# Optimization experiments

Hardware: AMD Instinct MI355X
Metric: run time of the kernel (lower is better)

The kernel has to match this reference:

```python
import jax, jax.numpy as jnp
import numpy as np

B, S, D, H = 2, 2048, 1024, 16
HD = D // H  # 64
NEG = 1.0e9


def setup_inputs() -> dict:
    key = jax.random.key(0)
    ks = jax.random.split(key, 9)
    scale = 1.0 / np.sqrt(D)
    return {
        "q_in": jax.random.normal(ks[0], (B, S, D), jnp.float32),
        "k_in": jax.random.normal(ks[1], (B, S, D), jnp.float32),
        "v_in": jax.random.normal(ks[2], (B, S, D), jnp.float32),
        "Wq": jax.random.normal(ks[3], (D, D), jnp.float32) * scale,
        "bq": jnp.zeros((D,), jnp.float32),
        "Wk": jax.random.normal(ks[4], (D, D), jnp.float32) * scale,
        "bk": jnp.zeros((D,), jnp.float32),
        "Wv": jax.random.normal(ks[5], (D, D), jnp.float32) * scale,
        "bv": jnp.zeros((D,), jnp.float32),
        "Wo": jax.random.normal(ks[6], (D, D), jnp.float32) * scale,
        "bo": jnp.zeros((D,), jnp.float32),
    }


def _split_heads(x):
    # [B,S,D] -> [B,H,S,HD]
    return x.reshape(B, S, H, HD).transpose(0, 2, 1, 3)


def reference(q_in, k_in, v_in, Wq, bq, Wk, bk, Wv, bv, Wo, bo):
    q = _split_heads(q_in @ Wq + bq)
    k = _split_heads(k_in @ Wk + bk)
    v = _split_heads(v_in @ Wv + bv)
    # scaled dot-product attention with additive causal mask (use_causal_mask=True)
    scores = jnp.einsum("bhqd,bhkd->bhqk", q, k) / jnp.sqrt(jnp.float32(HD))
    causal = jnp.tril(jnp.ones((S, S), jnp.float32))  # band_part(ones, -1, 0)
    scores = scores + (causal - 1.0) * NEG
    weights = jax.nn.softmax(scores, axis=-1)
    attn = jnp.einsum("bhqk,bhkd->bhqd", weights, v)
    concat = attn.transpose(0, 2, 1, 3).reshape(B, S, D)
    return concat @ Wo + bo
```

## Files before the change

### kernel.cpp

```cpp
#include <hip/hip_runtime.h>

#define B_  2
#define S_  2048
#define D_  1024
#define H_  16
#define HD_ 64
#define MM  (B_ * S_)

typedef __bf16 bf16;
typedef __attribute__((ext_vector_type(8))) __bf16 bf16x8;
typedef __attribute__((ext_vector_type(4))) __bf16 bf16x4;
typedef __attribute__((ext_vector_type(4))) float  f32x4;

__device__ inline float exp2g(float x) { return __builtin_amdgcn_exp2f(x); }

__device__ inline bf16x8 load8(const bf16* p) { return *(const bf16x8*)p; }
__device__ inline bf16x8 load8(const float* p) {
  float4 a = *(const float4*)p;
  float4 b = *(const float4*)(p + 4);
  bf16x8 r;
  r[0] = (bf16)a.x; r[1] = (bf16)a.y; r[2] = (bf16)a.z; r[3] = (bf16)a.w;
  r[4] = (bf16)b.x; r[5] = (bf16)b.y; r[6] = (bf16)b.z; r[7] = (bf16)b.w;
  return r;
}

__device__ inline void gld16(void* lds, const void* g) {
  __builtin_amdgcn_global_load_lds(
      (const __attribute__((address_space(1))) unsigned int*)g,
      (__attribute__((address_space(3))) unsigned int*)lds, 16, 0, 0);
}

__global__ __launch_bounds__(256) void transpose_w(
    const float* __restrict__ W0, const float* __restrict__ W1,
    const float* __restrict__ W2, const float* __restrict__ W3,
    bf16* __restrict__ T0, bf16* __restrict__ T1,
    bf16* __restrict__ T2, bf16* __restrict__ T3,
    const float* __restrict__ X0, const float* __restrict__ X1,
    const float* __restrict__ X2,
    bf16* __restrict__ Y0, bf16* __restrict__ Y1, bf16* __restrict__ Y2) {
  const int z = blockIdx.z;
  if (z >= 4) {
    const int p = z - 4, t = p >> 2;
    const float* src = t == 0 ? X0 : t == 1 ? X1 : X2;
    bf16* dst = t == 0 ? Y0 : t == 1 ? Y1 : Y2;
    long base = ((long)(p & 3) << 20) +
                (long)(blockIdx.y * 32 + blockIdx.x) * 1024 + threadIdx.x * 4;
    float4 v = *(const float4*)&src[base];
    bf16x4 o4;
    o4[0] = (bf16)v.x; o4[1] = (bf16)v.y; o4[2] = (bf16)v.z; o4[3] = (bf16)v.w;
    *(bf16x4*)&dst[base] = o4;
    return;
  }
  __shared__ bf16 t[32][40];
  const float* in = z == 0 ? W0 : z == 1 ? W1 : z == 2 ? W2 : W3;
  bf16* out = z == 0 ? T0 : z == 1 ? T1 : z == 2 ? T2 : T3;
  const int tx = threadIdx.x & 31;
  const int ty = threadIdx.x >> 5;
  const int r0 = blockIdx.y * 32, c0 = blockIdx.x * 32;
#pragma unroll
  for (int j = 0; j < 32; j += 8)
    t[ty + j][tx] = (bf16)in[(long)(r0 + ty + j) * D_ + (c0 + tx)];
  __syncthreads();
#pragma unroll
  for (int j = 0; j < 32; j += 8)
    out[(long)(c0 + ty + j) * D_ + (r0 + tx)] = t[tx][ty + j];
}

__global__ __launch_bounds__(256) void transpose_v64(const bf16* __restrict__ V,
                                                     bf16* __restrict__ VT) {
  __shared__ bf16 t[64][72];
  const int tid = threadIdx.x;
  const int s0 = blockIdx.x * 64;
  const int bh = blockIdx.y;
  const int b = bh >> 4, h = bh & 15;
  const bf16* ip = V + (long)b * S_ * D_ + h * HD_;
  bf16* op = VT + (long)bh * HD_ * S_;
#pragma unroll
  for (int i = 0; i < 2; ++i) {
    int c = tid + i * 256;
    int r = c >> 3, cc = (c & 7) * 8;
    *(bf16x8*)&t[r][cc] = *(const bf16x8*)&ip[(long)(s0 + r) * D_ + cc];
  }
  __syncthreads();
#pragma unroll
  for (int i = 0; i < 2; ++i) {
    int c = tid + i * 256;
    int d = c >> 3, sc = (c & 7) * 8;
    bf16x8 v;
#pragma unroll
    for (int j = 0; j < 8; ++j) v[j] = t[sc + j][d];
    *(bf16x8*)&op[(long)d * S_ + s0 + sc] = v;
  }
}

template <typename AT, typename OT>
__global__ __launch_bounds__(256) void gemm_bt_dma(
    const AT* __restrict__ A0, const AT* __restrict__ A1, const AT* __restrict__ A2,
    const bf16* __restrict__ B0, const bf16* __restrict__ B1, const bf16* __restrict__ B2,
    const float* __restrict__ c0, const float* __restrict__ c1, const float* __restrict__ c2,
    OT* __restrict__ C0, OT* __restrict__ C1, OT* __restrict__ C2,
    int M, int N, int K) {
  __shared__ bf16 lA[128][32];
  __shared__ bf16 lB[128][32];
  const int z = blockIdx.z;
  const AT*    A    = z == 0 ? A0 : z == 1 ? A1 : A2;
  const bf16*  Bt   = z == 0 ? B0 : z == 1 ? B1 : B2;
  const float* bias = z == 0 ? c0 : z == 1 ? c1 : c2;
  OT*          C    = z == 0 ? C0 : z == 1 ? C1 : C2;

  const int tid = threadIdx.x;
  const int lane = tid & 63, wave = tid >> 6;
  const int quad = lane >> 4, l16 = lane & 15;
  const int bm = blockIdx.y * 128, bn = blockIdx.x * 128;
  const int wm = (wave >> 1) * 64, wn = (wave & 1) * 64;

  f32x4 acc[4][4] = {};

  for (int k0 = 0; k0 < K; k0 += 32) {
    __syncthreads();
#pragma unroll
    for (int i = 0; i < 2; ++i) {
      const int nbase = wave * 128 + i * 64;
      const int n = nbase + lane;
      const int row = n >> 2, kc = (n & 3) * 8;
      gld16(&lB[0][0] + (long)nbase * 8, &Bt[(long)(bn + row) * K + k0 + kc]);
      if constexpr (__is_same(AT, bf16))
        gld16(&lA[0][0] + (long)nbase * 8, &A[(long)(bm + row) * K + k0 + kc]);
    }
    if constexpr (!__is_same(AT, bf16)) {
#pragma unroll
      for (int i = 0; i < 2; ++i) {
        int c = tid + i * 256;
        int row = c >> 2, kc = (c & 3) * 8;
        *(bf16x8*)&lA[row][kc] = load8(&A[(long)(bm + row) * K + k0 + kc]);
      }
    }
    __syncthreads();
    bf16x8 af[4], bfr[4];
#pragma unroll
    for (int i = 0; i < 4; ++i) {
      af[i]  = *(const bf16x8*)&lA[wm + i * 16 + l16][quad * 8];
      bfr[i] = *(const bf16x8*)&lB[wn + i * 16 + l16][quad * 8];
    }
#pragma unroll
    for (int mi = 0; mi < 4; ++mi)
#pragma unroll
      for (int ni = 0; ni < 4; ++ni)
        acc[mi][ni] = __builtin_amdgcn_mfma_f32_16x16x32_bf16(af[mi], bfr[ni],
                                                              acc[mi][ni], 0, 0, 0);
  }

#pragma unroll
  for (int mi = 0; mi < 4; ++mi)
#pragma unroll
    for (int ni = 0; ni < 4; ++ni) {
      int col = bn + wn + ni * 16 + l16;
      float bv = bias[col];
#pragma unroll
      for (int r = 0; r < 4; ++r) {
        int row = bm + wm + mi * 16 + quad * 4 + r;
        C[(long)row * N + col] = (OT)(acc[mi][ni][r] + bv);
      }
    }
}

__global__ __launch_bounds__(256) void gemm_bt_64(const bf16* __restrict__ A,
                                                  const bf16* __restrict__ Bt,
                                                  const float* __restrict__ bias,
                                                  float* __restrict__ C,
                                                  int M, int N, int K) {
  __shared__ bf16 lA[128][32];
  __shared__ bf16 lB[64][32];
  const int tid = threadIdx.x;
  const int lane = tid & 63, wave = tid >> 6;
  const int quad = lane >> 4, l16 = lane & 15;
  const int bm = blockIdx.y * 128, bn = blockIdx.x * 64;
  const int wm = (wave >> 1) * 64, wn = (wave & 1) * 32;

  f32x4 acc[4][2] = {};

  for (int k0 = 0; k0 < K; k0 += 32) {
    __syncthreads();
#pragma unroll
    for (int i = 0; i < 2; ++i) {
      const int nbase = wave * 128 + i * 64;
      const int n = nbase + lane;
      const int row = n >> 2, kc = (n & 3) * 8;
      gld16(&lA[0][0] + (long)nbase * 8, &A[(long)(bm + row) * K + k0 + kc]);
    }
    {
      const int nbase = wave * 64;
      const int n = nbase + lane;
      const int row = n >> 2, kc = (n & 3) * 8;
      gld16(&lB[0][0] + (long)nbase * 8, &Bt[(long)(bn + row) * K + k0 + kc]);
    }
    __syncthreads();
    bf16x8 af[4], bfr[2];
#pragma unroll
    for (int i = 0; i < 4; ++i)
      af[i] = *(const bf16x8*)&lA[wm + i * 16 + l16][quad * 8];
#pragma unroll
    for (int i = 0; i < 2; ++i)
      bfr[i] = *(const bf16x8*)&lB[wn + i * 16 + l16][quad * 8];
#pragma unroll
    for (int mi = 0; mi < 4; ++mi)
#pragma unroll
      for (int ni = 0; ni < 2; ++ni)
        acc[mi][ni] = __builtin_amdgcn_mfma_f32_16x16x32_bf16(af[mi], bfr[ni],
                                                              acc[mi][ni], 0, 0, 0);
  }

#pragma unroll
  for (int mi = 0; mi < 4; ++mi)
#pragma unroll
    for (int ni = 0; ni < 2; ++ni) {
      int col = bn + wn + ni * 16 + l16;
      float bv = bias[col];
#pragma unroll
      for (int r = 0; r < 4; ++r) {
        int row = bm + wm + mi * 16 + quad * 4 + r;
        C[(long)row * N + col] = acc[mi][ni][r] + bv;
      }
    }
}

#define SCALE_LOG2E 0.1803368801111244f

__device__ inline void attn_step7(bool diag, int qloc, int kh, int quad,
                                  int l16,
                                  const bf16 (*lKb)[64], const bf16 (*lVb)[64],
                                  bf16 (*lpw)[72], const bf16x8* aq,
                                  f32x4* o, float& l_s) {
  const int sw = l16 & 7;
  f32x4 s[2];
#pragma unroll
  for (int i = 0; i < 2; ++i) {
    const int ni = 2 * kh + i;
    f32x4 a = {};
#pragma unroll
    for (int c = 0; c < 2; ++c) {
      bf16x8 kf = *(const bf16x8*)&lKb[ni * 16 + l16][((c * 4 + quad) ^ sw) * 8];
      a = __builtin_amdgcn_mfma_f32_16x16x32_bf16(kf, aq[c], a, 0, 0, 0);
    }
    s[i] = a * SCALE_LOG2E;
  }
  if (diag) {
#pragma unroll
    for (int i = 0; i < 2; ++i)
#pragma unroll
      for (int r = 0; r < 4; ++r)
        if ((2 * kh + i) * 16 + quad * 4 + r > qloc) s[i][r] = -1e9f;
  }
  float rs = 0.f;
#pragma unroll
  for (int i = 0; i < 2; ++i) {
    bf16x4 p4;
#pragma unroll
    for (int r = 0; r < 4; ++r) {
      float p = exp2g(s[i][r]);
      p4[r] = (bf16)p;
      rs += p;
    }
    *(bf16x4*)&lpw[l16][(2 * kh + i) * 16 + quad * 4] = p4;
  }
  l_s += rs;
  bf16x8 ap = *(const bf16x8*)&lpw[l16][kh * 32 + quad * 8];
#pragma unroll
  for (int di = 0; di < 4; ++di) {
    bf16x8 vf = *(const bf16x8*)&lVb[di * 16 + l16][((kh * 4 + quad) ^ sw) * 8];
    o[di] = __builtin_amdgcn_mfma_f32_16x16x32_bf16(vf, ap, o[di], 0, 0, 0);
  }
}

__device__ inline void store_o(bf16* Ob, int qrow, int lane, int quad, int l16,
                               bf16 (*lpw)[72], const f32x4* o, float l_s) {
  float rs = l_s;
  rs += __shfl_xor(rs, 16);
  rs += __shfl_xor(rs, 32);
  const float inv = 1.0f / rs;
#pragma unroll
  for (int di = 0; di < 4; ++di) {
    bf16x4 p4;
#pragma unroll
    for (int r = 0; r < 4; ++r) p4[r] = (bf16)(o[di][r] * inv);
    *(bf16x4*)&lpw[l16][di * 16 + quad * 4] = p4;
  }
  const int q = lane >> 2, db = (lane & 3) * 16;
  bf16x8 v0 = *(const bf16x8*)&lpw[q][db];
  bf16x8 v1 = *(const bf16x8*)&lpw[q][db + 8];
  *(bf16x8*)&Ob[(long)(qrow + q) * D_ + db] = v0;
  *(bf16x8*)&Ob[(long)(qrow + q) * D_ + db + 8] = v1;
}

__global__ __launch_bounds__(512) void flash_attn7(const bf16* __restrict__ Q,
                                                   const bf16* __restrict__ K,
                                                   const bf16* __restrict__ VT,
                                                   bf16* __restrict__ O) {
  __shared__ bf16 lKV[2][2][64][64];
  __shared__ bf16 lp[8][16][72];
  __shared__ float lsum[512];
  const int tid = threadIdx.x;
  const int lane = tid & 63, wave = tid >> 6;
  const int quad = lane >> 4, l16 = lane & 15;
  const int qgroup = wave & 3, kh = wave >> 2;
  const int x = blockIdx.x, bh = blockIdx.y;
  const int qtA = x, qtB = 31 - x;
  const int b = bh >> 4, h = bh & 15;
  const bf16* Qb = Q + (long)b * S_ * D_ + h * HD_;
  const bf16* Kb = K + (long)b * S_ * D_ + h * HD_;
  const bf16* Vb = VT + (long)bh * HD_ * S_;
  const int qrowA = qtA * 64 + qgroup * 16;
  const int qrowB = qtB * 64 + qgroup * 16;
  const int qloc = qgroup * 16 + l16;

  bf16x8 aqA[2], aqB[2];
#pragma unroll
  for (int c = 0; c < 2; ++c) {
    aqA[c] = *(const bf16x8*)&Qb[(long)(qrowA + l16) * D_ + c * 32 + quad * 8];
    aqB[c] = *(const bf16x8*)&Qb[(long)(qrowB + l16) * D_ + c * 32 + quad * 8];
  }

  f32x4 oA[4] = {}, oB[4] = {};
  float lA = 0.f, lB = 0.f;

  const int srow = tid >> 3, scol = tid & 7;
  const int swcol = (scol ^ (srow & 7)) * 8;

  bf16x8 kreg, vreg;
  kreg = *(const bf16x8*)&Kb[(long)srow * D_ + scol * 8];
  vreg = *(const bf16x8*)&Vb[(long)srow * S_ + scol * 8];
  *(bf16x8*)&lKV[0][0][srow][swcol] = kreg;
  *(bf16x8*)&lKV[1][0][srow][swcol] = vreg;
  __syncthreads();

  for (int t = 0; t <= 32; ++t) {
    const int p = t & 1;
    if (t < 32) {
      const int g = (t + 1 <= qtA) ? (t + 1) : (t - qtA);
      const long k0 = (long)g * 64;
      kreg = *(const bf16x8*)&Kb[(k0 + srow) * D_ + scol * 8];
      vreg = *(const bf16x8*)&Vb[(long)srow * S_ + k0 + scol * 8];
    }
    if (t <= qtA)
      attn_step7(t == qtA, qloc, kh, quad, l16, lKV[0][p], lKV[1][p],
                 lp[qgroup], aqA, oA, lA);
    else
      attn_step7(t == 32, qloc, kh, quad, l16, lKV[0][p], lKV[1][p],
                 lp[qgroup], aqB, oB, lB);
    if (t < 32) {
      *(bf16x8*)&lKV[0][1 - p][srow][swcol] = kreg;
      *(bf16x8*)&lKV[1][1 - p][srow][swcol] = vreg;
      __syncthreads();
    }
  }

  __syncthreads();
  float* scrO = (float*)lKV;
  const int pairid = qgroup * 64 + lane;
  if (kh == 1) {
#pragma unroll
    for (int di = 0; di < 4; ++di)
#pragma unroll
      for (int r = 0; r < 4; ++r)
        scrO[pairid * 16 + di * 4 + r] = oA[di][r];
    lsum[pairid] = lA;
  } else {
#pragma unroll
    for (int di = 0; di < 4; ++di)
#pragma unroll
      for (int r = 0; r < 4; ++r)
        scrO[4096 + pairid * 16 + di * 4 + r] = oB[di][r];
    lsum[256 + pairid] = lB;
  }
  __syncthreads();
  bf16* Ob = O + (long)b * S_ * D_ + h * HD_;
  if (kh == 0) {
#pragma unroll
    for (int di = 0; di < 4; ++di)
#pragma unroll
      for (int r = 0; r < 4; ++r)
        oA[di][r] += scrO[pairid * 16 + di * 4 + r];
    lA += lsum[pairid];
    store_o(Ob, qrowA, lane, quad, l16, lp[wave], oA, lA);
  } else {
#pragma unroll
    for (int di = 0; di < 4; ++di)
#pragma unroll
      for (int r = 0; r < 4; ++r)
        oB[di][r] += scrO[4096 + pairid * 16 + di * 4 + r];
    lB += lsum[256 + pairid];
    store_o(Ob, qrowB, lane, quad, l16, lp[wave], oB, lB);
  }
}

extern "C" void kernel_launch(void* const* d_in, const int* in_sizes, int n_in,
                              void* d_out, int out_size, void* d_ws, size_t ws_size,
                              hipStream_t stream) {
  (void)in_sizes; (void)n_in; (void)out_size;
  const float* q_in = (const float*)d_in[0];
  const float* k_in = (const float*)d_in[1];
  const float* v_in = (const float*)d_in[2];
  const float* Wq   = (const float*)d_in[3];
  const float* bq   = (const float*)d_in[4];
  const float* Wk   = (const float*)d_in[5];
  const float* bk   = (const float*)d_in[6];
  const float* Wv   = (const float*)d_in[7];
  const float* bv   = (const float*)d_in[8];
  const float* Wo   = (const float*)d_in[9];
  const float* bo   = (const float*)d_in[10];
  float* out = (float*)d_out;

  bf16* ws = (bf16*)d_ws;
  const size_t WSZ = (size_t)D_ * D_;
  const size_t TSZ = (size_t)B_ * S_ * D_;
  bf16* WqT = ws;
  bf16* WkT = WqT + WSZ;
  bf16* WvT = WkT + WSZ;
  bf16* WoT = WvT + WSZ;
  bf16* Qp  = WoT + WSZ;
  bf16* Kp  = Qp + TSZ;
  bf16* Vp  = Kp + TSZ;
  bf16* VTp = Vp + TSZ;
  bf16* Ap  = VTp + TSZ;
  bf16* Xq  = VTp;
  bf16* Xk  = Ap;
  bf16* Xv  = Ap + TSZ;
  const bool pre = ws_size >= (4 * WSZ + 6 * TSZ) * sizeof(bf16);

  dim3 blk(256);
  transpose_w<<<dim3(32, 32, pre ? 16 : 4), blk, 0, stream>>>(
      Wq, Wk, Wv, Wo, WqT, WkT, WvT, WoT, q_in, k_in, v_in, Xq, Xk, Xv);

  if (pre)
    gemm_bt_dma<bf16, bf16><<<dim3(8, 32, 3), blk, 0, stream>>>(
        Xq, Xk, Xv, WqT, WkT, WvT, bq, bk, bv, Qp, Kp, Vp, MM, D_, D_);
  else
    gemm_bt_dma<float, bf16><<<dim3(8, 32, 3), blk, 0, stream>>>(
        q_in, k_in, v_in, WqT, WkT, WvT, bq, bk, bv, Qp, Kp, Vp, MM, D_, D_);

  transpose_v64<<<dim3(S_ / 64, B_ * H_), blk, 0, stream>>>(Vp, VTp);

  flash_attn7<<<dim3(16, B_ * H_), dim3(512), 0, stream>>>(Qp, Kp, VTp, Ap);

  gemm_bt_64<<<dim3(16, 32), blk, 0, stream>>>(Ap, WoT, bo, out, MM, D_, D_);
}
```

Before: 231.3 us.

## Replace paired causal query tiles with one tile per block, longest first

The flash attention kernel stops pairing query tiles x and 31-x in one block and gives each block a single 64-row query tile. Blocks are reversed so the longest causal rows launch first, and the grid doubles to 32x32 blocks. This aims to raise parallelism and occupancy on the many compute units and simplifies the register state. In exchange, per-block work becomes uneven and the block count and per-block setup overhead double.

```diff
diff --git a/kernel.cpp b/kernel.cpp
--- a/kernel.cpp
+++ b/kernel.cpp
@@ -226,7 +226,7 @@
 
 #define SCALE_LOG2E 0.1803368801111244f
 
-__device__ inline void attn_step7(bool diag, int qloc, int kh, int quad,
+__device__ inline void attn_step8(bool diag, int qloc, int kh, int quad,
                                   int l16,
                                   const bf16 (*lKb)[64], const bf16 (*lVb)[64],
                                   bf16 (*lpw)[72], const bf16x8* aq,
@@ -292,36 +292,33 @@
   *(bf16x8*)&Ob[(long)(qrow + q) * D_ + db + 8] = v1;
 }
 
-__global__ __launch_bounds__(512) void flash_attn7(const bf16* __restrict__ Q,
+__global__ __launch_bounds__(512) void flash_attn8(const bf16* __restrict__ Q,
                                                    const bf16* __restrict__ K,
                                                    const bf16* __restrict__ VT,
                                                    bf16* __restrict__ O) {
   __shared__ bf16 lKV[2][2][64][64];
   __shared__ bf16 lp[8][16][72];
-  __shared__ float lsum[512];
+  __shared__ float lsum[256];
   const int tid = threadIdx.x;
   const int lane = tid & 63, wave = tid >> 6;
   const int quad = lane >> 4, l16 = lane & 15;
   const int qgroup = wave & 3, kh = wave >> 2;
-  const int x = blockIdx.x, bh = blockIdx.y;
-  const int qtA = x, qtB = 31 - x;
+  const int qt = 31 - blockIdx.x;
+  const int bh = blockIdx.y;
   const int b = bh >> 4, h = bh & 15;
   const bf16* Qb = Q + (long)b * S_ * D_ + h * HD_;
   const bf16* Kb = K + (long)b * S_ * D_ + h * HD_;
   const bf16* Vb = VT + (long)bh * HD_ * S_;
-  const int qrowA = qtA * 64 + qgroup * 16;
-  const int qrowB = qtB * 64 + qgroup * 16;
+  const int qrow = qt * 64 + qgroup * 16;
   const int qloc = qgroup * 16 + l16;
 
-  bf16x8 aqA[2], aqB[2];
-#pragma unroll
-  for (int c = 0; c < 2; ++c) {
-    aqA[c] = *(const bf16x8*)&Qb[(long)(qrowA + l16) * D_ + c * 32 + quad * 8];
-    aqB[c] = *(const bf16x8*)&Qb[(long)(qrowB + l16) * D_ + c * 32 + quad * 8];
-  }
-
-  f32x4 oA[4] = {}, oB[4] = {};
-  float lA = 0.f, lB = 0.f;
+  bf16x8 aq[2];
+#pragma unroll
+  for (int c = 0; c < 2; ++c)
+    aq[c] = *(const bf16x8*)&Qb[(long)(qrow + l16) * D_ + c * 32 + quad * 8];
+
+  f32x4 o[4] = {};
+  float l_s = 0.f;
 
   const int srow = tid >> 3, scol = tid & 7;
   const int swcol = (scol ^ (srow & 7)) * 8;
@@ -333,21 +330,16 @@
   *(bf16x8*)&lKV[1][0][srow][swcol] = vreg;
   __syncthreads();
 
-  for (int t = 0; t <= 32; ++t) {
+  for (int t = 0; t <= qt; ++t) {
     const int p = t & 1;
-    if (t < 32) {
-      const int g = (t + 1 <= qtA) ? (t + 1) : (t - qtA);
-      const long k0 = (long)g * 64;
+    if (t < qt) {
+      const long k0 = (long)(t + 1) * 64;
       kreg = *(const bf16x8*)&Kb[(k0 + srow) * D_ + scol * 8];
       vreg = *(const bf16x8*)&Vb[(long)srow * S_ + k0 + scol * 8];
     }
-    if (t <= qtA)
-      attn_step7(t == qtA, qloc, kh, quad, l16, lKV[0][p], lKV[1][p],
-                 lp[qgroup], aqA, oA, lA);
-    else
-      attn_step7(t == 32, qloc, kh, quad, l16, lKV[0][p], lKV[1][p],
-                 lp[qgroup], aqB, oB, lB);
-    if (t < 32) {
+    attn_step8(t == qt, qloc, kh, quad, l16, lKV[0][p], lKV[1][p],
+               lp[qgroup], aq, o, l_s);
+    if (t < qt) {
       *(bf16x8*)&lKV[0][1 - p][srow][swcol] = kreg;
       *(bf16x8*)&lKV[1][1 - p][srow][swcol] = vreg;
       __syncthreads();
@@ -362,34 +354,19 @@
     for (int di = 0; di < 4; ++di)
 #pragma unroll
       for (int r = 0; r < 4; ++r)
-        scrO[pairid * 16 + di * 4 + r] = oA[di][r];
-    lsum[pairid] = lA;
-  } else {
+        scrO[pairid * 16 + di * 4 + r] = o[di][r];
+    lsum[pairid] = l_s;
+  }
+  __syncthreads();
+  if (kh == 0) {
 #pragma unroll
     for (int di = 0; di < 4; ++di)
 #pragma unroll
       for (int r = 0; r < 4; ++r)
-        scrO[4096 + pairid * 16 + di * 4 + r] = oB[di][r];
-    lsum[256 + pairid] = lB;
-  }
-  __syncthreads();
-  bf16* Ob = O + (long)b * S_ * D_ + h * HD_;
-  if (kh == 0) {
-#pragma unroll
-    for (int di = 0; di < 4; ++di)
-#pragma unroll
-      for (int r = 0; r < 4; ++r)
-        oA[di][r] += scrO[pairid * 16 + di * 4 + r];
-    lA += lsum[pairid];
-    store_o(Ob, qrowA, lane, quad, l16, lp[wave], oA, lA);
-  } else {
-#pragma unroll
-    for (int di = 0; di < 4; ++di)
-#pragma unroll
-      for (int r = 0; r < 4; ++r)
-        oB[di][r] += scrO[4096 + pairid * 16 + di * 4 + r];
-    lB += lsum[256 + pairid];
-    store_o(Ob, qrowB, lane, quad, l16, lp[wave], oB, lB);
+        o[di][r] += scrO[pairid * 16 + di * 4 + r];
+    l_s += lsum[pairid];
+    bf16* Ob = O + (long)b * S_ * D_ + h * HD_;
+    store_o(Ob, qrow, lane, quad, l16, lp[wave], o, l_s);
   }
 }
 
@@ -440,7 +417,7 @@
 
   transpose_v64<<<dim3(S_ / 64, B_ * H_), blk, 0, stream>>>(Vp, VTp);
 
-  flash_attn7<<<dim3(16, B_ * H_), dim3(512), 0, stream>>>(Qp, Kp, VTp, Ap);
+  flash_attn8<<<dim3(32, B_ * H_), dim3(512), 0, stream>>>(Qp, Kp, VTp, Ap);
 
   gemm_bt_64<<<dim3(16, 32), blk, 0, stream>>>(Ap, WoT, bo, out, MM, D_, D_);
 }
```

Measured after the change: 244.9 us. 1.06x slower.
